# Optimization experiments

Measured on AMD Instinct MI355X. Metric: run time of the kernel, lower is better.

## Reference

```python
import jax, jax.numpy as jnp
import numpy as np

B, T, C = 2, 2048, 1024
H = 16
HS = C // H
EPS = 1e-5


def layernorm(x, g, b):
    mu = jnp.mean(x, axis=-1, keepdims=True)
    var = jnp.var(x, axis=-1, keepdims=True)
    return (x - mu) * jax.lax.rsqrt(var + EPS) * g + b


def setup_inputs() -> dict:
    key = jax.random.key(0)
    ks = jax.random.split(key, 12)
    s_in = 1.0 / np.sqrt(C)
    s_ff = 1.0 / np.sqrt(4 * C)
    return {
        "x": jax.random.normal(ks[0], (B, T, C), jnp.float32),
        "Wq": jax.random.normal(ks[1], (H, C, HS), jnp.float32) * s_in,
        "Wk": jax.random.normal(ks[2], (H, C, HS), jnp.float32) * s_in,
        "Wv": jax.random.normal(ks[3], (H, C, HS), jnp.float32) * s_in,
        "Wo": jax.random.normal(ks[4], (C, C), jnp.float32) * s_in,
        "bo": jnp.zeros((C,), jnp.float32),
        "W1": jax.random.normal(ks[5], (C, 4 * C), jnp.float32) * s_in,
        "b1": jnp.zeros((4 * C,), jnp.float32),
        "W2": jax.random.normal(ks[6], (4 * C, C), jnp.float32) * s_ff,
        "b2": jnp.zeros((C,), jnp.float32),
        "g1": jnp.ones((C,), jnp.float32),
        "be1": jnp.zeros((C,), jnp.float32),
        "g2": jnp.ones((C,), jnp.float32),
        "be2": jnp.zeros((C,), jnp.float32),
    }


def reference(x, Wq, Wk, Wv, Wo, bo, W1, b1, W2, b2, g1, be1, g2, be2):
    # x: [B,T,C]. Dropout is identity (eval mode).
    x = layernorm(x, g1, be1)
    # --- multi-head causal self-attention (per-source: scale by C**-0.5, NOT head_size) ---
    q = jnp.einsum("btc,hcd->bhtd", x, Wq)
    k = jnp.einsum("btc,hcd->bhtd", x, Wk)
    v = jnp.einsum("btc,hcd->bhtd", x, Wv)
    scores = jnp.einsum("bhtd,bhsd->bhts", q, k) * (C ** -0.5)  # [B,H,T,T]
    causal = jnp.tril(jnp.ones((T, T), bool))
    scores = jnp.where(causal, scores, -jnp.inf)
    wei = jax.nn.softmax(scores, axis=-1)
    attn = jnp.einsum("bhts,bhsd->bhtd", wei, v)
    attn = attn.transpose(0, 2, 1, 3).reshape(B, T, C)  # concat heads on last dim
    sa = attn @ Wo + bo
    x = x + sa
    # --- MLP with second pre-op LayerNorm ---
    x = layernorm(x, g2, be2)
    h = jax.nn.relu(x @ W1 + b1)
    x = x + (h @ W2 + b2)
    return x
```

## Files before the change

### kernel.cpp

```cpp
#include <hip/hip_runtime.h>
#include <hip/hip_bf16.h>
#include <math.h>

#define B_ 2
#define T_ 2048
#define C_ 1024
#define H_ 16
#define HS_ 64
#define N_ROWS (B_*T_)
#define MB (1024*1024)

typedef __attribute__((ext_vector_type(8))) short bf16x8;
typedef __attribute__((ext_vector_type(8))) unsigned short u16x8;
typedef __attribute__((ext_vector_type(4))) float floatx4;

static __device__ __forceinline__ unsigned short f2bf(float f) {
  union { float f; unsigned u; } v; v.f = f;
  unsigned r = v.u + 0x7fff + ((v.u >> 16) & 1);
  return (unsigned short)(r >> 16);
}
static __device__ __forceinline__ float bf2f(unsigned short s) {
  union { unsigned u; float f; } v; v.u = ((unsigned)s) << 16;
  return v.f;
}

__global__ __launch_bounds__(256) void ln_kernel(
    const float* __restrict__ x, const float* __restrict__ g,
    const float* __restrict__ b, unsigned short* __restrict__ outb)
{
  const int row = blockIdx.x;
  const int tid = threadIdx.x;
  const float* xr = x + (size_t)row * C_;
  float4 xv = *reinterpret_cast<const float4*>(xr + tid * 4);
  float s  = xv.x + xv.y + xv.z + xv.w;
  float ss = xv.x*xv.x + xv.y*xv.y + xv.z*xv.z + xv.w*xv.w;
  #pragma unroll
  for (int off = 32; off > 0; off >>= 1) {
    s  += __shfl_down(s, off, 64);
    ss += __shfl_down(ss, off, 64);
  }
  __shared__ float rs[4], rss[4];
  __shared__ float smu, srstd;
  if ((tid & 63) == 0) { rs[tid >> 6] = s; rss[tid >> 6] = ss; }
  __syncthreads();
  if (tid == 0) {
    float S  = rs[0] + rs[1] + rs[2] + rs[3];
    float SS = rss[0] + rss[1] + rss[2] + rss[3];
    float mu  = S * (1.0f / C_);
    float var = SS * (1.0f / C_) - mu * mu;
    smu = mu; srstd = rsqrtf(var + 1e-5f);
  }
  __syncthreads();
  const float mu = smu, rstd = srstd;
  float4 gv = *reinterpret_cast<const float4*>(g + tid * 4);
  float4 bv = *reinterpret_cast<const float4*>(b + tid * 4);
  union { unsigned long long ll; unsigned short s[4]; } o;
  o.s[0] = f2bf((xv.x - mu) * rstd * gv.x + bv.x);
  o.s[1] = f2bf((xv.y - mu) * rstd * gv.y + bv.y);
  o.s[2] = f2bf((xv.z - mu) * rstd * gv.z + bv.z);
  o.s[3] = f2bf((xv.w - mu) * rstd * gv.w + bv.w);
  *reinterpret_cast<unsigned long long*>(outb + (size_t)row * C_ + tid * 4) = o.ll;
}

__global__ __launch_bounds__(256) void transpose_cast(
    const float* __restrict__ in, unsigned short* __restrict__ out, int R, int Cc)
{
  __shared__ float tile[32][33];
  const int bz = blockIdx.z;
  in  += (size_t)bz * R * Cc;
  out += (size_t)bz * R * Cc;
  const int tx = threadIdx.x & 31;
  const int ty = threadIdx.x >> 5;
  const int c0 = blockIdx.x * 32, r0 = blockIdx.y * 32;
  #pragma unroll
  for (int j = 0; j < 4; ++j)
    tile[ty + j*8][tx] = in[(size_t)(r0 + ty + j*8) * Cc + c0 + tx];
  __syncthreads();
  #pragma unroll
  for (int j = 0; j < 4; ++j)
    out[(size_t)(c0 + ty + j*8) * R + r0 + tx] = f2bf(tile[tx][ty + j*8]);
}

__global__ __launch_bounds__(256) void transpose_cast_qkv(
    const float* __restrict__ Wq, const float* __restrict__ Wk,
    const float* __restrict__ Wv, unsigned short* __restrict__ out)
{
  __shared__ float tile[32][33];
  const int z = blockIdx.z;
  const int which = z >> 4, h = z & 15;
  const float* in = (which == 0 ? Wq : which == 1 ? Wk : Wv) + (size_t)h * C_ * HS_;
  unsigned short* dst = out + (size_t)z * C_ * HS_;
  const int tx = threadIdx.x & 31;
  const int ty = threadIdx.x >> 5;
  const int c0 = blockIdx.x * 32, r0 = blockIdx.y * 32;
  #pragma unroll
  for (int j = 0; j < 4; ++j)
    tile[ty + j*8][tx] = in[(size_t)(r0 + ty + j*8) * HS_ + c0 + tx];
  __syncthreads();
  #pragma unroll
  for (int j = 0; j < 4; ++j)
    dst[(size_t)(c0 + ty + j*8) * C_ + r0 + tx] = f2bf(tile[tx][ty + j*8]);
}

template<int TNB, bool OUTBF16, bool RELU, bool HASB, bool HASRES>
__global__ __launch_bounds__(256) void gemm_bf16(
    const unsigned short* __restrict__ A,
    const unsigned short* __restrict__ Bt,
    const float* __restrict__ bias,
    const unsigned short* __restrict__ res,
    void* __restrict__ Cout,
    int M, int N, int K)
{
  constexpr int NT = TNB / 32;
  constexpr int WN = TNB / 2;
  constexpr int LOADS = 4 + 2 * (TNB / 64);
  __shared__ unsigned short As[2][2][128 * 32];
  __shared__ unsigned short Bs[2][2][TNB * 32];
  const int tid  = threadIdx.x;
  const int lane = tid & 63;
  const int wave = tid >> 6;
  const int wm = wave & 1, wn = wave >> 1;
  const int m0 = blockIdx.x * 128, n0 = blockIdx.y * TNB;

  const int lrow = lane >> 2;
  const int lcol = (lane & 3) * 8;
  const int fr = lane & 15;
  const int fq = lane >> 4;

  floatx4 acc[4][NT] = {};

  const unsigned short* Aw = A  + (size_t)m0 * K;
  const unsigned short* Bw = Bt + (size_t)n0 * K;

  auto STAGE = [&](int bb, int k0) {
    #pragma unroll
    for (int half = 0; half < 2; ++half) {
      #pragma unroll
      for (int i = 0; i < 2; ++i) {
        const int rbase = i * 64 + wave * 16;
        const unsigned short* gp =
            Aw + (size_t)(rbase + lrow) * K + k0 + half * 32 + lcol;
        __builtin_amdgcn_global_load_lds(
            (const __attribute__((address_space(1))) void*)gp,
            (__attribute__((address_space(3))) void*)(As[bb][half] + rbase * 32),
            16, 0, 0);
      }
      #pragma unroll
      for (int i = 0; i < TNB / 64; ++i) {
        const int rbase = i * 64 + wave * 16;
        const unsigned short* gp =
            Bw + (size_t)(rbase + lrow) * K + k0 + half * 32 + lcol;
        __builtin_amdgcn_global_load_lds(
            (const __attribute__((address_space(1))) void*)gp,
            (__attribute__((address_space(3))) void*)(Bs[bb][half] + rbase * 32),
            16, 0, 0);
      }
    }
  };

  auto COMPUTE = [&](int bb) {
    #pragma unroll
    for (int half = 0; half < 2; ++half) {
      bf16x8 af[4], bfr[NT];
      #pragma unroll
      for (int t = 0; t < 4; ++t)
        af[t]  = *reinterpret_cast<const bf16x8*>(
            As[bb][half] + (wm*64 + t*16 + fr)*32 + fq*8);
      #pragma unroll
      for (int t = 0; t < NT; ++t)
        bfr[t] = *reinterpret_cast<const bf16x8*>(
            Bs[bb][half] + (wn*WN + t*16 + fr)*32 + fq*8);
      #pragma unroll
      for (int mt = 0; mt < 4; ++mt)
        #pragma unroll
        for (int nt = 0; nt < NT; ++nt)
          acc[mt][nt] = __builtin_amdgcn_mfma_f32_16x16x32_bf16(
              af[mt], bfr[nt], acc[mt][nt], 0, 0, 0);
    }
  };

  STAGE(0, 0);
  int bb = 0;
  for (int k0 = 64; k0 < K; k0 += 64) {
    STAGE(bb ^ 1, k0);
    asm volatile("s_waitcnt vmcnt(%0)" :: "n"(LOADS) : "memory");
    __builtin_amdgcn_s_barrier();
    COMPUTE(bb);
    __builtin_amdgcn_s_barrier();
    bb ^= 1;
  }
  asm volatile("s_waitcnt vmcnt(0)" ::: "memory");
  __builtin_amdgcn_s_barrier();
  COMPUTE(bb);

  #pragma unroll
  for (int nt = 0; nt < NT; ++nt) {
    const int col = n0 + wn*WN + nt*16 + fr;
    const float bv = HASB ? bias[col] : 0.0f;
    #pragma unroll
    for (int mt = 0; mt < 4; ++mt) {
      #pragma unroll
      for (int r = 0; r < 4; ++r) {
        const int row = m0 + wm*64 + mt*16 + fq*4 + r;
        float v = acc[mt][nt][r] + bv;
        if (RELU) v = v > 0.0f ? v : 0.0f;
        if (HASRES) v += bf2f(res[(size_t)row * N + col]);
        if (OUTBF16) ((unsigned short*)Cout)[(size_t)row * N + col] = f2bf(v);
        else         ((float*)Cout)[(size_t)row * N + col] = v;
      }
    }
  }
}

template<int TNB, int SPLITS>
__global__ __launch_bounds__(256) void gemm_splitk(
    const unsigned short* __restrict__ A,
    const unsigned short* __restrict__ Bt,
    unsigned short* __restrict__ Cpart,
    int M, int N, int Kfull)
{
  constexpr int NT = TNB / 32;
  constexpr int WN = TNB / 2;
  constexpr int LOADS = 4 + 2 * (TNB / 64);
  __shared__ unsigned short As[2][2][128 * 32];
  __shared__ unsigned short Bs[2][2][TNB * 32];
  const int tid  = threadIdx.x;
  const int lane = tid & 63;
  const int wave = tid >> 6;
  const int wm = wave & 1, wn = wave >> 1;
  const int m0 = blockIdx.x * 128, n0 = blockIdx.y * TNB;
  const int z  = blockIdx.z;
  const int Kh = Kfull / SPLITS;

  const int lrow = lane >> 2;
  const int lcol = (lane & 3) * 8;
  const int fr = lane & 15;
  const int fq = lane >> 4;

  floatx4 acc[4][NT] = {};

  const unsigned short* Aw = A  + (size_t)m0 * Kfull + (size_t)z * Kh;
  const unsigned short* Bw = Bt + (size_t)n0 * Kfull + (size_t)z * Kh;
  unsigned short* Cw = Cpart + (size_t)z * M * N;

  auto STAGE = [&](int bb, int k0) {
    #pragma unroll
    for (int half = 0; half < 2; ++half) {
      #pragma unroll
      for (int i = 0; i < 2; ++i) {
        const int rbase = i * 64 + wave * 16;
        const unsigned short* gp =
            Aw + (size_t)(rbase + lrow) * Kfull + k0 + half * 32 + lcol;
        __builtin_amdgcn_global_load_lds(
            (const __attribute__((address_space(1))) void*)gp,
            (__attribute__((address_space(3))) void*)(As[bb][half] + rbase * 32),
            16, 0, 0);
      }
      #pragma unroll
      for (int i = 0; i < TNB / 64; ++i) {
        const int rbase = i * 64 + wave * 16;
        const unsigned short* gp =
            Bw + (size_t)(rbase + lrow) * Kfull + k0 + half * 32 + lcol;
        __builtin_amdgcn_global_load_lds(
            (const __attribute__((address_space(1))) void*)gp,
            (__attribute__((address_space(3))) void*)(Bs[bb][half] + rbase * 32),
            16, 0, 0);
      }
    }
  };

  auto COMPUTE = [&](int bb) {
    #pragma unroll
    for (int half = 0; half < 2; ++half) {
      bf16x8 af[4], bfr[NT];
      #pragma unroll
      for (int t = 0; t < 4; ++t)
        af[t]  = *reinterpret_cast<const bf16x8*>(
            As[bb][half] + (wm*64 + t*16 + fr)*32 + fq*8);
      #pragma unroll
      for (int t = 0; t < NT; ++t)
        bfr[t] = *reinterpret_cast<const bf16x8*>(
            Bs[bb][half] + (wn*WN + t*16 + fr)*32 + fq*8);
      #pragma unroll
      for (int mt = 0; mt < 4; ++mt)
        #pragma unroll
        for (int nt = 0; nt < NT; ++nt)
          acc[mt][nt] = __builtin_amdgcn_mfma_f32_16x16x32_bf16(
              af[mt], bfr[nt], acc[mt][nt], 0, 0, 0);
    }
  };

  STAGE(0, 0);
  int bb = 0;
  for (int k0 = 64; k0 < Kh; k0 += 64) {
    STAGE(bb ^ 1, k0);
    asm volatile("s_waitcnt vmcnt(%0)" :: "n"(LOADS) : "memory");
    __builtin_amdgcn_s_barrier();
    COMPUTE(bb);
    __builtin_amdgcn_s_barrier();
    bb ^= 1;
  }
  asm volatile("s_waitcnt vmcnt(0)" ::: "memory");
  __builtin_amdgcn_s_barrier();
  COMPUTE(bb);

  #pragma unroll
  for (int nt = 0; nt < NT; ++nt) {
    const int col = n0 + wn*WN + nt*16 + fr;
    #pragma unroll
    for (int mt = 0; mt < 4; ++mt)
      #pragma unroll
      for (int r = 0; r < 4; ++r) {
        const int row = m0 + wm*64 + mt*16 + fq*4 + r;
        Cw[(size_t)row * N + col] = f2bf(acc[mt][nt][r]);
      }
  }
}

template<int SPLITS>
__global__ __launch_bounds__(256) void splitk_reduce(
    const unsigned short* __restrict__ p,
    const float* __restrict__ bias, const unsigned short* __restrict__ res,
    float* __restrict__ out)
{
  const size_t i = ((size_t)blockIdx.x * 256 + threadIdx.x) * 4;
  const size_t MN = (size_t)N_ROWS * C_;
  float4 bv = *reinterpret_cast<const float4*>(bias + (i & (size_t)(C_ - 1)));
  float acc[4] = {bv.x, bv.y, bv.z, bv.w};
  {
    const unsigned short* rp = res + i;
    #pragma unroll
    for (int j = 0; j < 4; ++j) acc[j] += bf2f(rp[j]);
  }
  #pragma unroll
  for (int z = 0; z < SPLITS; ++z) {
    const unsigned short* pp = p + (size_t)z * MN + i;
    #pragma unroll
    for (int j = 0; j < 4; ++j) acc[j] += bf2f(pp[j]);
  }
  float4 o; o.x = acc[0]; o.y = acc[1]; o.z = acc[2]; o.w = acc[3];
  *reinterpret_cast<float4*>(out + i) = o;
}

__global__ __launch_bounds__(256) void v_transpose(
    const unsigned short* __restrict__ qkv, unsigned short* __restrict__ vt)
{
  __shared__ __align__(16) unsigned short sT[64][72];
  const int st = blockIdx.x;
  const int bh = blockIdx.y;
  const int b = bh >> 4, h = bh & 15;
  const int t = threadIdx.x;
  const int r = t >> 2, c0 = (t & 3) * 16;
  const unsigned short* src =
      qkv + (size_t)(b * T_ + st * 64 + r) * 3072 + 2048 + h * 64 + c0;
  *(u16x8*)&sT[r][c0]     = *(const u16x8*)src;
  *(u16x8*)&sT[r][c0 + 8] = *(const u16x8*)(src + 8);
  __syncthreads();
  const int d = t >> 2, sc = (t & 3) * 16;
  unsigned short v[16];
  #pragma unroll
  for (int j = 0; j < 16; ++j) v[j] = sT[sc + j][d];
  unsigned short* dst = vt + ((size_t)bh * 64 + d) * (size_t)T_ + st * 64 + sc;
  *(uint4*)dst       = *(uint4*)&v[0];
  *(uint4*)(dst + 8) = *(uint4*)&v[8];
}

__global__ __launch_bounds__(256, 3) void attn_mfma(
    const unsigned short* __restrict__ qkv,
    const unsigned short* __restrict__ vt,
    unsigned short* __restrict__ out)
{
  const int bh = blockIdx.x;
  const int qt = (int)(gridDim.y - 1) - (int)blockIdx.y;
  const int b = bh >> 4, h = bh & 15;
  const int tid = threadIdx.x;
  const int w = tid >> 6;
  const int lane = tid & 63;
  const int l15 = lane & 15, fq = lane >> 4;
  const int t0 = qt * 64;
  const int q_row = t0 + w * 16 + l15;

  __shared__ __align__(16) unsigned short sK [128][72];
  __shared__ __align__(16) unsigned short sVt[64][136];
  __shared__ __align__(16) unsigned short sP [64][136];

  const float c1 = 1.4426950408889634f / 32.0f;

  bf16x8 aq[2];
  {
    const unsigned short* qp = qkv + (size_t)(b*T_ + q_row)*3072 + h*HS_ + fq*8;
    aq[0] = *(const bf16x8*)qp;
    aq[1] = *(const bf16x8*)(qp + 32);
  }

  const int nks = (qt >> 1) + 1;

  const int kr = tid >> 1, kc = (tid & 1) * 32;
  const int vr = tid >> 2, vc = (tid & 3) * 32;
  const unsigned short* kp0 =
      qkv + (size_t)(b*T_ + kr)*3072 + C_ + h*HS_ + kc;
  const unsigned short* vp0 =
      vt + ((size_t)bh*64 + vr)*(size_t)T_ + vc;

  u16x8 kg0, kg1, kg2, kg3, vg0, vg1, vg2, vg3;
  kg0 = *(const u16x8*)kp0;      kg1 = *(const u16x8*)(kp0 + 8);
  kg2 = *(const u16x8*)(kp0+16); kg3 = *(const u16x8*)(kp0 + 24);
  vg0 = *(const u16x8*)vp0;      vg1 = *(const u16x8*)(vp0 + 8);
  vg2 = *(const u16x8*)(vp0+16); vg3 = *(const u16x8*)(vp0 + 24);
  *(u16x8*)&sK [kr][kc]      = kg0; *(u16x8*)&sK [kr][kc + 8]  = kg1;
  *(u16x8*)&sK [kr][kc + 16] = kg2; *(u16x8*)&sK [kr][kc + 24] = kg3;
  *(u16x8*)&sVt[vr][vc]      = vg0; *(u16x8*)&sVt[vr][vc + 8]  = vg1;
  *(u16x8*)&sVt[vr][vc + 16] = vg2; *(u16x8*)&sVt[vr][vc + 24] = vg3;

  floatx4 oacc[4] = {};
  float m_s = -3.0e38f, l_s = 0.0f;

  #pragma unroll 1
  for (int ks = 0; ks < nks; ++ks) {
    asm volatile("s_waitcnt lgkmcnt(0)" ::: "memory");
    __builtin_amdgcn_s_barrier();

    if (ks + 1 < nks) {
      const unsigned short* kp = kp0 + (size_t)(ks + 1) * (128 * 3072);
      kg0 = *(const u16x8*)kp;        kg1 = *(const u16x8*)(kp + 8);
      kg2 = *(const u16x8*)(kp + 16); kg3 = *(const u16x8*)(kp + 24);
      const unsigned short* vp = vp0 + (ks + 1) * 128;
      vg0 = *(const u16x8*)vp;        vg1 = *(const u16x8*)(vp + 8);
      vg2 = *(const u16x8*)(vp + 16); vg3 = *(const u16x8*)(vp + 24);
    }

    floatx4 stacc[8] = {};
    __builtin_amdgcn_s_setprio(1);
    #pragma unroll
    for (int st = 0; st < 8; ++st) {
      bf16x8 ka = *(const bf16x8*)&sK[st*16 + l15][fq*8];
      bf16x8 kb = *(const bf16x8*)&sK[st*16 + l15][32 + fq*8];
      stacc[st] = __builtin_amdgcn_mfma_f32_16x16x32_bf16(ka, aq[0], stacc[st], 0, 0, 0);
      stacc[st] = __builtin_amdgcn_mfma_f32_16x16x32_bf16(kb, aq[1], stacc[st], 0, 0, 0);
    }
    __builtin_amdgcn_s_setprio(0);

    if (ks == nks - 1) {
      const int sbase = ks*128 + fq*4;
      #pragma unroll
      for (int st = 0; st < 8; ++st)
        #pragma unroll
        for (int r = 0; r < 4; ++r)
          if (sbase + st*16 + r > q_row) stacc[st][r] = -3.0e38f;
    }

    float mx = -3.0e38f;
    #pragma unroll
    for (int st = 0; st < 8; ++st)
      #pragma unroll
      for (int r = 0; r < 4; ++r) mx = fmaxf(mx, stacc[st][r]);
    mx = fmaxf(mx, __shfl_xor(mx, 16, 64));
    mx = fmaxf(mx, __shfl_xor(mx, 32, 64));

    float mnew;
    if (__all((mx - m_s) * c1 <= 8.0f)) {
      mnew = m_s;
    } else {
      mnew = fmaxf(m_s, mx);
      const float alpha = __builtin_amdgcn_exp2f((m_s - mnew) * c1);
      #pragma unroll
      for (int r = 0; r < 4; ++r) {
        const float ar = __shfl(alpha, fq*4 + r, 64);
        #pragma unroll
        for (int dt = 0; dt < 4; ++dt) oacc[dt][r] *= ar;
      }
      l_s *= alpha;
      m_s = mnew;
    }

    const float mc = mnew * c1;
    float sum = 0.0f;
    #pragma unroll
    for (int st = 0; st < 8; ++st) {
      unsigned pu[4];
      #pragma unroll
      for (int r = 0; r < 4; ++r) {
        const float p = __builtin_amdgcn_exp2f(stacc[st][r] * c1 - mc);
        sum += p;
        union { float f; unsigned u; } cv; cv.f = p;
        pu[r] = cv.u + 0x8000u;
      }
      const unsigned lo = __builtin_amdgcn_perm(pu[1], pu[0], 0x07060302u);
      const unsigned hi = __builtin_amdgcn_perm(pu[3], pu[2], 0x07060302u);
      *(unsigned long long*)&sP[w*16 + l15][st*16 + fq*4] =
          ((unsigned long long)hi << 32) | lo;
    }
    sum += __shfl_xor(sum, 16, 64);
    sum += __shfl_xor(sum, 32, 64);
    l_s += sum;

    __builtin_amdgcn_s_setprio(1);
    #pragma unroll
    for (int c = 0; c < 4; ++c) {
      bf16x8 ap = *(const bf16x8*)&sP[w*16 + l15][c*32 + fq*8];
      #pragma unroll
      for (int dt = 0; dt < 4; ++dt) {
        bf16x8 bv = *(const bf16x8*)&sVt[dt*16 + l15][c*32 + fq*8];
        oacc[dt] = __builtin_amdgcn_mfma_f32_16x16x32_bf16(ap, bv, oacc[dt], 0, 0, 0);
      }
    }
    __builtin_amdgcn_s_setprio(0);

    asm volatile("s_waitcnt lgkmcnt(0)" ::: "memory");
    __builtin_amdgcn_s_barrier();
    if (ks + 1 < nks) {
      *(u16x8*)&sK [kr][kc]      = kg0; *(u16x8*)&sK [kr][kc + 8]  = kg1;
      *(u16x8*)&sK [kr][kc + 16] = kg2; *(u16x8*)&sK [kr][kc + 24] = kg3;
      *(u16x8*)&sVt[vr][vc]      = vg0; *(u16x8*)&sVt[vr][vc + 8]  = vg1;
      *(u16x8*)&sVt[vr][vc + 16] = vg2; *(u16x8*)&sVt[vr][vc + 24] = vg3;
    }
  }

  #pragma unroll
  for (int r = 0; r < 4; ++r) {
    const float il = 1.0f / __shfl(l_s, fq*4 + r, 64);
    const int q = t0 + w*16 + fq*4 + r;
    #pragma unroll
    for (int dt = 0; dt < 4; ++dt)
      out[(size_t)(b*T_ + q)*C_ + h*HS_ + dt*16 + l15] = f2bf(oacc[dt][r] * il);
  }
}

extern "C" void kernel_launch(void* const* d_in, const int* in_sizes, int n_in,
                              void* d_out, int out_size, void* d_ws, size_t ws_size,
                              hipStream_t stream)
{
  const float* x   = (const float*)d_in[0];
  const float* Wq  = (const float*)d_in[1];
  const float* Wk  = (const float*)d_in[2];
  const float* Wv  = (const float*)d_in[3];
  const float* Wo  = (const float*)d_in[4];
  const float* bo  = (const float*)d_in[5];
  const float* W1  = (const float*)d_in[6];
  const float* b1  = (const float*)d_in[7];
  const float* W2  = (const float*)d_in[8];
  const float* b2  = (const float*)d_in[9];
  const float* g1  = (const float*)d_in[10];
  const float* be1 = (const float*)d_in[11];
  const float* g2  = (const float*)d_in[12];
  const float* be2 = (const float*)d_in[13];
  float* out = (float*)d_out;

  char* ws = (char*)d_ws;
  unsigned short* BtQKV = (unsigned short*)(ws + (size_t) 0*MB);
  unsigned short* BtWo  = (unsigned short*)(ws + (size_t) 6*MB);
  unsigned short* BtW1  = (unsigned short*)(ws + (size_t) 8*MB);
  unsigned short* BtW2  = (unsigned short*)(ws + (size_t)16*MB);
  unsigned short* lnb   = (unsigned short*)(ws + (size_t)24*MB);
  unsigned short* qkvb  = (unsigned short*)(ws + (size_t)32*MB);
  unsigned short* vtb   = (unsigned short*)(ws + (size_t)56*MB);
  unsigned short* attnb = (unsigned short*)(ws + (size_t)64*MB);
  float*          x2    = (float*)         (ws + (size_t)32*MB);
  unsigned short* hb    = (unsigned short*)(ws + (size_t)32*MB);
  unsigned short* pk2   = (unsigned short*)(ws + (size_t)64*MB);

  dim3 blk(256);

  transpose_cast_qkv<<<dim3(HS_/32, C_/32, 3*H_), blk, 0, stream>>>(Wq, Wk, Wv, BtQKV);
  transpose_cast<<<dim3(C_/32,  C_/32, 1),  blk, 0, stream>>>(Wo, BtWo, C_, C_);
  transpose_cast<<<dim3(4*C_/32,C_/32, 1),  blk, 0, stream>>>(W1, BtW1, C_, 4*C_);
  transpose_cast<<<dim3(C_/32,4*C_/32, 1),  blk, 0, stream>>>(W2, BtW2, 4*C_, C_);

  ln_kernel<<<dim3(N_ROWS), blk, 0, stream>>>(x, g1, be1, lnb);

  gemm_bf16<128,true,false,false,false><<<dim3(N_ROWS/128, 3072/128), blk, 0, stream>>>(
      lnb, BtQKV, nullptr, nullptr, qkvb, N_ROWS, 3072, C_);

  v_transpose<<<dim3(T_/64, B_*H_), blk, 0, stream>>>(qkvb, vtb);

  attn_mfma<<<dim3(B_*H_, T_/64), blk, 0, stream>>>(qkvb, vtb, attnb);

  gemm_bf16<64,false,false,true,true><<<dim3(N_ROWS/128, C_/64), blk, 0, stream>>>(
      attnb, BtWo, bo, lnb, x2, N_ROWS, C_, C_);

  ln_kernel<<<dim3(N_ROWS), blk, 0, stream>>>(x2, g2, be2, lnb);

  gemm_bf16<128,true,true,true,false><<<dim3(N_ROWS/128, 4*C_/128), blk, 0, stream>>>(
      lnb, BtW1, b1, nullptr, hb, N_ROWS, 4*C_, C_);

  gemm_splitk<128,2><<<dim3(N_ROWS/128, C_/128, 2), blk, 0, stream>>>(
      hb, BtW2, pk2, N_ROWS, C_, 4*C_);

  splitk_reduce<2><<<dim3((N_ROWS * C_) / (256 * 4)), blk, 0, stream>>>(
      pk2, b2, lnb, out);
}
```

Measured before the change: 342.9 us.

## Add 256x256-tile 512-thread GEMM with 4-stage LDS pipeline for QKV, W1, W2

Introduces a new GEMM kernel using 256x256 output tiles with 8 waves, a 4-deep global_load_lds ring buffer with swizzled LDS layout, and split-phase MFMA with setprio. It replaces the 128-tile GEMMs for the QKV projection, the W1 projection and the split-K W2 projection, with W2 now split four ways and reduced by splitk_reduce<4>. The aim is more data reuse per tile and better latency hiding. The cost is fewer blocks (e.g. 16x12 for QKV), so CU occupancy and wave quantization may suffer, along with more partial-sum traffic for the 4-way split.

```diff
diff --git a/kernel.cpp b/kernel.cpp
--- a/kernel.cpp
+++ b/kernel.cpp
@@ -102,6 +102,133 @@
     dst[(size_t)(c0 + ty + j*8) * C_ + r0 + tx] = f2bf(tile[tx][ty + j*8]);
 }
 
+template<bool RELU, bool HASB>
+__global__ __launch_bounds__(512, 2) void gemm256(
+    const unsigned short* __restrict__ A,
+    const unsigned short* __restrict__ Bt,
+    const float* __restrict__ bias,
+    unsigned short* __restrict__ Cout,
+    int M, int N, int Kfull, int Kh)
+{
+  __shared__ __align__(16) unsigned short Asl[4 * 8192];
+  __shared__ __align__(16) unsigned short Bsl[4 * 8192];
+  const int tid = threadIdx.x;
+  const int w = tid >> 6, l = tid & 63;
+  const int wm = w & 1, wn = w >> 1;
+  const int fr = l & 15, fq = l >> 4;
+  const int m0 = blockIdx.x * 256, n0 = blockIdx.y * 256;
+  const int z = blockIdx.z;
+
+  const unsigned short* Aw = A  + (size_t)m0 * Kfull + (size_t)z * Kh;
+  const unsigned short* Bw = Bt + (size_t)n0 * Kfull + (size_t)z * Kh;
+  unsigned short* Cw = Cout + (size_t)z * M * N;
+
+  const int g    = ((l & 3) - ((l >> 3) & 3)) & 3;
+  const int srow = w * 16 + (l >> 2);
+  const unsigned short* ga0 = Aw + (size_t)srow * Kfull + g * 8;
+  const unsigned short* ga1 = ga0 + (size_t)128 * Kfull;
+  const unsigned short* gb0 = Bw + (size_t)srow * Kfull + g * 8;
+  const unsigned short* gb1 = gb0 + (size_t)128 * Kfull;
+  unsigned short* da0 = Asl + w * 512;
+  unsigned short* db0 = Bsl + w * 512;
+
+  const int Qmax = (Kh >> 5) - 1;
+
+  auto SA = [&](int q) {
+    unsigned short* d = da0 + (q & 3) * 8192;
+    __builtin_amdgcn_global_load_lds(
+        (const __attribute__((address_space(1))) void*)(ga0 + q * 32),
+        (__attribute__((address_space(3))) void*)d, 16, 0, 0);
+    __builtin_amdgcn_global_load_lds(
+        (const __attribute__((address_space(1))) void*)(ga1 + q * 32),
+        (__attribute__((address_space(3))) void*)(d + 4096), 16, 0, 0);
+  };
+  auto SB = [&](int q) {
+    unsigned short* d = db0 + (q & 3) * 8192;
+    __builtin_amdgcn_global_load_lds(
+        (const __attribute__((address_space(1))) void*)(gb0 + q * 32),
+        (__attribute__((address_space(3))) void*)d, 16, 0, 0);
+    __builtin_amdgcn_global_load_lds(
+        (const __attribute__((address_space(1))) void*)(gb1 + q * 32),
+        (__attribute__((address_space(3))) void*)(d + 4096), 16, 0, 0);
+  };
+
+  const int slot8 = ((fq + (fr >> 1)) & 3) * 8;
+  const int aoff = (wm * 128 + fr) * 32 + slot8;
+  const int boff = (wn * 64  + fr) * 32 + slot8;
+
+  floatx4 acc[8][4] = {};
+
+  SA(0); SB(0);
+  if (Qmax >= 1) { SA(1); SB(1); }
+  if (Qmax >= 2) { SA(2); SB(2); }
+  asm volatile("s_waitcnt vmcnt(8)" ::: "memory");
+  __builtin_amdgcn_s_barrier();
+
+  #pragma unroll 1
+  for (int q = 0; q <= Qmax; ++q) {
+    const unsigned short* Ar = Asl + (q & 3) * 8192;
+    const unsigned short* Br = Bsl + (q & 3) * 8192;
+    const bool st = (q + 3 <= Qmax);
+
+    bf16x8 af[4], bfr[4];
+    #pragma unroll
+    for (int mf = 0; mf < 4; ++mf)
+      af[mf] = *(const bf16x8*)(Ar + aoff + mf * 512);
+    #pragma unroll
+    for (int nf = 0; nf < 4; ++nf)
+      bfr[nf] = *(const bf16x8*)(Br + boff + nf * 512);
+    if (st) SA(q + 3);
+    __builtin_amdgcn_s_barrier();
+    asm volatile("s_waitcnt lgkmcnt(0)" ::: "memory");
+    __builtin_amdgcn_s_setprio(1);
+    #pragma unroll
+    for (int mf = 0; mf < 4; ++mf)
+      #pragma unroll
+      for (int nf = 0; nf < 4; ++nf)
+        acc[mf][nf] = __builtin_amdgcn_mfma_f32_16x16x32_bf16(
+            af[mf], bfr[nf], acc[mf][nf], 0, 0, 0);
+    __builtin_amdgcn_s_setprio(0);
+    __builtin_amdgcn_s_barrier();
+
+    bf16x8 af2[4];
+    #pragma unroll
+    for (int mf = 0; mf < 4; ++mf)
+      af2[mf] = *(const bf16x8*)(Ar + aoff + (4 + mf) * 512);
+    if (st) SB(q + 3);
+    if (q + 3 <= Qmax)        { asm volatile("s_waitcnt vmcnt(8)" ::: "memory"); }
+    else if (q + 2 == Qmax)   { asm volatile("s_waitcnt vmcnt(4)" ::: "memory"); }
+    else if (q + 1 == Qmax)   { asm volatile("s_waitcnt vmcnt(0)" ::: "memory"); }
+    __builtin_amdgcn_s_barrier();
+    asm volatile("s_waitcnt lgkmcnt(0)" ::: "memory");
+    __builtin_amdgcn_s_setprio(1);
+    #pragma unroll
+    for (int mf = 0; mf < 4; ++mf)
+      #pragma unroll
+      for (int nf = 0; nf < 4; ++nf)
+        acc[4 + mf][nf] = __builtin_amdgcn_mfma_f32_16x16x32_bf16(
+            af2[mf], bfr[nf], acc[4 + mf][nf], 0, 0, 0);
+    __builtin_amdgcn_s_setprio(0);
+    __builtin_amdgcn_s_barrier();
+  }
+
+  #pragma unroll
+  for (int nf = 0; nf < 4; ++nf) {
+    const int col = n0 + wn * 64 + nf * 16 + fr;
+    const float bv = HASB ? bias[col] : 0.0f;
+    #pragma unroll
+    for (int mf = 0; mf < 8; ++mf) {
+      #pragma unroll
+      for (int r = 0; r < 4; ++r) {
+        const int row = m0 + wm * 128 + mf * 16 + fq * 4 + r;
+        float v = acc[mf][nf][r] + bv;
+        if (RELU) v = v > 0.0f ? v : 0.0f;
+        Cw[(size_t)row * N + col] = f2bf(v);
+      }
+    }
+  }
+}
+
 template<int TNB, bool OUTBF16, bool RELU, bool HASB, bool HASRES>
 __global__ __launch_bounds__(256) void gemm_bf16(
     const unsigned short* __restrict__ A,
@@ -209,111 +336,6 @@
         else         ((float*)Cout)[(size_t)row * N + col] = v;
       }
     }
-  }
-}
-
-template<int TNB, int SPLITS>
-__global__ __launch_bounds__(256) void gemm_splitk(
-    const unsigned short* __restrict__ A,
-    const unsigned short* __restrict__ Bt,
-    unsigned short* __restrict__ Cpart,
-    int M, int N, int Kfull)
-{
-  constexpr int NT = TNB / 32;
-  constexpr int WN = TNB / 2;
-  constexpr int LOADS = 4 + 2 * (TNB / 64);
-  __shared__ unsigned short As[2][2][128 * 32];
-  __shared__ unsigned short Bs[2][2][TNB * 32];
-  const int tid  = threadIdx.x;
-  const int lane = tid & 63;
-  const int wave = tid >> 6;
-  const int wm = wave & 1, wn = wave >> 1;
-  const int m0 = blockIdx.x * 128, n0 = blockIdx.y * TNB;
-  const int z  = blockIdx.z;
-  const int Kh = Kfull / SPLITS;
-
-  const int lrow = lane >> 2;
-  const int lcol = (lane & 3) * 8;
-  const int fr = lane & 15;
-  const int fq = lane >> 4;
-
-  floatx4 acc[4][NT] = {};
-
-  const unsigned short* Aw = A  + (size_t)m0 * Kfull + (size_t)z * Kh;
-  const unsigned short* Bw = Bt + (size_t)n0 * Kfull + (size_t)z * Kh;
-  unsigned short* Cw = Cpart + (size_t)z * M * N;
-
-  auto STAGE = [&](int bb, int k0) {
-    #pragma unroll
-    for (int half = 0; half < 2; ++half) {
-      #pragma unroll
-      for (int i = 0; i < 2; ++i) {
-        const int rbase = i * 64 + wave * 16;
-        const unsigned short* gp =
-            Aw + (size_t)(rbase + lrow) * Kfull + k0 + half * 32 + lcol;
-        __builtin_amdgcn_global_load_lds(
-            (const __attribute__((address_space(1))) void*)gp,
-            (__attribute__((address_space(3))) void*)(As[bb][half] + rbase * 32),
-            16, 0, 0);
-      }
-      #pragma unroll
-      for (int i = 0; i < TNB / 64; ++i) {
-        const int rbase = i * 64 + wave * 16;
-        const unsigned short* gp =
-            Bw + (size_t)(rbase + lrow) * Kfull + k0 + half * 32 + lcol;
-        __builtin_amdgcn_global_load_lds(
-            (const __attribute__((address_space(1))) void*)gp,
-            (__attribute__((address_space(3))) void*)(Bs[bb][half] + rbase * 32),
-            16, 0, 0);
-      }
-    }
-  };
-
-  auto COMPUTE = [&](int bb) {
-    #pragma unroll
-    for (int half = 0; half < 2; ++half) {
-      bf16x8 af[4], bfr[NT];
-      #pragma unroll
-      for (int t = 0; t < 4; ++t)
-        af[t]  = *reinterpret_cast<const bf16x8*>(
-            As[bb][half] + (wm*64 + t*16 + fr)*32 + fq*8);
-      #pragma unroll
-      for (int t = 0; t < NT; ++t)
-        bfr[t] = *reinterpret_cast<const bf16x8*>(
-            Bs[bb][half] + (wn*WN + t*16 + fr)*32 + fq*8);
-      #pragma unroll
-      for (int mt = 0; mt < 4; ++mt)
-        #pragma unroll
-        for (int nt = 0; nt < NT; ++nt)
-          acc[mt][nt] = __builtin_amdgcn_mfma_f32_16x16x32_bf16(
-              af[mt], bfr[nt], acc[mt][nt], 0, 0, 0);
-    }
-  };
-
-  STAGE(0, 0);
-  int bb = 0;
-  for (int k0 = 64; k0 < Kh; k0 += 64) {
-    STAGE(bb ^ 1, k0);
-    asm volatile("s_waitcnt vmcnt(%0)" :: "n"(LOADS) : "memory");
-    __builtin_amdgcn_s_barrier();
-    COMPUTE(bb);
-    __builtin_amdgcn_s_barrier();
-    bb ^= 1;
-  }
-  asm volatile("s_waitcnt vmcnt(0)" ::: "memory");
-  __builtin_amdgcn_s_barrier();
-  COMPUTE(bb);
-
-  #pragma unroll
-  for (int nt = 0; nt < NT; ++nt) {
-    const int col = n0 + wn*WN + nt*16 + fr;
-    #pragma unroll
-    for (int mt = 0; mt < 4; ++mt)
-      #pragma unroll
-      for (int r = 0; r < 4; ++r) {
-        const int row = m0 + wm*64 + mt*16 + fq*4 + r;
-        Cw[(size_t)row * N + col] = f2bf(acc[mt][nt][r]);
-      }
   }
 }
 
@@ -557,9 +579,10 @@
   unsigned short* attnb = (unsigned short*)(ws + (size_t)64*MB);
   float*          x2    = (float*)         (ws + (size_t)32*MB);
   unsigned short* hb    = (unsigned short*)(ws + (size_t)32*MB);
-  unsigned short* pk2   = (unsigned short*)(ws + (size_t)64*MB);
+  unsigned short* pk4   = (unsigned short*)(ws + (size_t)64*MB);
 
   dim3 blk(256);
+  dim3 blk512(512);
 
   transpose_cast_qkv<<<dim3(HS_/32, C_/32, 3*H_), blk, 0, stream>>>(Wq, Wk, Wv, BtQKV);
   transpose_cast<<<dim3(C_/32,  C_/32, 1),  blk, 0, stream>>>(Wo, BtWo, C_, C_);
@@ -568,8 +591,8 @@
 
   ln_kernel<<<dim3(N_ROWS), blk, 0, stream>>>(x, g1, be1, lnb);
 
-  gemm_bf16<128,true,false,false,false><<<dim3(N_ROWS/128, 3072/128), blk, 0, stream>>>(
-      lnb, BtQKV, nullptr, nullptr, qkvb, N_ROWS, 3072, C_);
+  gemm256<false,false><<<dim3(N_ROWS/256, 3072/256, 1), blk512, 0, stream>>>(
+      lnb, BtQKV, nullptr, qkvb, N_ROWS, 3072, C_, C_);
 
   v_transpose<<<dim3(T_/64, B_*H_), blk, 0, stream>>>(qkvb, vtb);
 
@@ -580,12 +603,12 @@
 
   ln_kernel<<<dim3(N_ROWS), blk, 0, stream>>>(x2, g2, be2, lnb);
 
-  gemm_bf16<128,true,true,true,false><<<dim3(N_ROWS/128, 4*C_/128), blk, 0, stream>>>(
-      lnb, BtW1, b1, nullptr, hb, N_ROWS, 4*C_, C_);
-
-  gemm_splitk<128,2><<<dim3(N_ROWS/128, C_/128, 2), blk, 0, stream>>>(
-      hb, BtW2, pk2, N_ROWS, C_, 4*C_);
-
-  splitk_reduce<2><<<dim3((N_ROWS * C_) / (256 * 4)), blk, 0, stream>>>(
-      pk2, b2, lnb, out);
-}
+  gemm256<true,true><<<dim3(N_ROWS/256, 4*C_/256, 1), blk512, 0, stream>>>(
+      lnb, BtW1, b1, hb, N_ROWS, 4*C_, C_, C_);
+
+  gemm256<false,false><<<dim3(N_ROWS/256, C_/256, 4), blk512, 0, stream>>>(
+      hb, BtW2, nullptr, pk4, N_ROWS, C_, 4*C_, C_);
+
+  splitk_reduce<4><<<dim3((N_ROWS * C_) / (256 * 4)), blk, 0, stream>>>(
+      pk4, b2, lnb, out);
+}
```

After: 342.9 us. No clear change (-0.0%).
